# Performance work log

Hardware: AMD Instinct MI355X
Metric: run time of the kernel (lower is better)

## Reference

```python
import jax, jax.numpy as jnp
import numpy as np

B, S, C = 512, 16384, 3
CLASS_W = jnp.array([1.23954983922, 5.3172413793, 192.75], dtype=jnp.float32)


def setup_inputs() -> dict:
    key = jax.random.key(0)
    kx, kc, kl = jax.random.split(key, 3)
    x = jax.random.normal(kx, (B, S, C), dtype=jnp.float32)
    # one-hot labels with a random valid prefix length per sample (>=1);
    # rows beyond the length are all-zero (the module's padding sentinel [0,0,0])
    classes = jax.random.randint(kc, (B, S), 0, C)                      # [B,S]
    lengths = jax.random.randint(kl, (B,), 1, S + 1)                    # [B], 1..S
    valid = jnp.arange(S)[None, :] < lengths[:, None]                   # [B,S] bool
    label = jax.nn.one_hot(classes, C, dtype=jnp.int64) * valid[:, :, None]
    return {"x": x, "label": label}


def reference(x, label):
    # padding_index scan: first all-zero label row ends the valid prefix
    nonzero = jnp.any(label != 0, axis=-1)                              # [B,S]
    valid = jnp.cumprod(nonzero.astype(jnp.int32), axis=1)              # [B,S] 0/1 prefix mask
    valid_f = valid.astype(x.dtype)

    # weighted soft-target cross entropy per token:
    #   l_t = -sum_c w_c * y_{t,c} * log_softmax(x_t)_c
    logp = jax.nn.log_softmax(x, axis=-1)                               # [B,S,C]
    tok_loss = -jnp.einsum('bsc,c,bsc->bs', label.astype(x.dtype), CLASS_W, logp)

    # per-sample: mean over the valid prefix (CrossEntropyLoss mean over N
    # tokens for probability targets), then sum over the batch (python loop +=)
    n_valid = jnp.sum(valid_f, axis=1)                                  # [B]
    per_sample = jnp.sum(tok_loss * valid_f, axis=1) / n_valid          # [B]
    loss = jnp.sum(per_sample)
    return loss
```

## Files before the change

kernel.cpp:

```cpp
#include <hip/hip_runtime.h>


#define NB      512
#define NS      16384
#define NSPLIT  4
#define RPB     (NS / NSPLIT)
#define NTH     512
#define GRP     (RPB / 4)

__device__ __forceinline__ float row_loss(float xa, float xb, float xc,
                                          int la, int lb, int lc) {
    const float w0 = 1.23954983922f, w1 = 5.3172413793f, w2 = 192.75f;
    float m   = fmaxf(fmaxf(xa, xb), xc);
    float lse = m + __logf(__expf(xa - m) + __expf(xb - m) + __expf(xc - m));
    return w0 * (float)la * (lse - xa)
         + w1 * (float)lb * (lse - xb)
         + w2 * (float)lc * (lse - xc);
}

__global__ __launch_bounds__(NTH) void ls_partial(
    const float* __restrict__ x, const int* __restrict__ lab,
    float* __restrict__ psum, int* __restrict__ pcnt)
{
    const int blk = blockIdx.x;
    const int b   = blk & (NB - 1);
    const int sp  = blk >> 9;
    const long long base = ((long long)b * NS + (long long)sp * RPB) * 3;
    const int*   lr = lab + base;
    const float* xr = x   + base;

    int f0 = lr[0], f1 = lr[1], f2 = lr[2];
    int e0 = lr[(RPB - 1) * 3], e1 = lr[(RPB - 1) * 3 + 1], e2 = lr[(RPB - 1) * 3 + 2];

    if ((f0 | f1 | f2) == 0) {
        if (threadIdx.x == 0) { psum[blk] = 0.0f; pcnt[blk] = 0; }
        return;
    }

    float sumA = 0.0f, sumB = 0.0f;
    int   cnt = 0;

    if ((e0 | e1 | e2) != 0) {
        const int g0 = threadIdx.x;
        const int g1 = threadIdx.x + NTH;
        const int4*   lp0 = (const int4*)lr + (size_t)g0 * 3;
        const int4*   lp1 = (const int4*)lr + (size_t)g1 * 3;
        const float4* xp0 = (const float4*)xr + (size_t)g0 * 3;
        const float4* xp1 = (const float4*)xr + (size_t)g1 * 3;

        int4   a0 = lp0[0], a1 = lp0[1], a2 = lp0[2];
        int4   b0 = lp1[0], b1 = lp1[1], b2 = lp1[2];
        float4 u0 = xp0[0], u1 = xp0[1], u2 = xp0[2];
        float4 v0 = xp1[0], v1 = xp1[1], v2 = xp1[2];

        sumA += row_loss(u0.x, u0.y, u0.z, a0.x, a0.y, a0.z);
        sumB += row_loss(u0.w, u1.x, u1.y, a0.w, a1.x, a1.y);
        sumA += row_loss(u1.z, u1.w, u2.x, a1.z, a1.w, a2.x);
        sumB += row_loss(u2.y, u2.z, u2.w, a2.y, a2.z, a2.w);
        sumA += row_loss(v0.x, v0.y, v0.z, b0.x, b0.y, b0.z);
        sumB += row_loss(v0.w, v1.x, v1.y, b0.w, b1.x, b1.y);
        sumA += row_loss(v1.z, v1.w, v2.x, b1.z, b1.w, b2.x);
        sumB += row_loss(v2.y, v2.z, v2.w, b2.y, b2.z, b2.w);
        cnt = 8;
    } else {
        for (int g = threadIdx.x; g < GRP; g += NTH) {
            const int4* lp = (const int4*)lr + (size_t)g * 3;
            int4 l0 = lp[0], l1 = lp[1], l2 = lp[2];
            int any = l0.x | l0.y | l0.z | l0.w |
                      l1.x | l1.y | l1.z | l1.w |
                      l2.x | l2.y | l2.z | l2.w;
            if (any == 0) continue;
            const float4* xp = (const float4*)xr + (size_t)g * 3;
            float4 x0 = xp[0], x1 = xp[1], x2 = xp[2];
            float xv[12] = {x0.x, x0.y, x0.z, x0.w,
                            x1.x, x1.y, x1.z, x1.w,
                            x2.x, x2.y, x2.z, x2.w};
            int   lv[12] = {l0.x, l0.y, l0.z, l0.w,
                            l1.x, l1.y, l1.z, l1.w,
                            l2.x, l2.y, l2.z, l2.w};
#pragma unroll
            for (int r = 0; r < 4; ++r) {
                int la = lv[3*r], lb = lv[3*r+1], lc = lv[3*r+2];
                if ((la | lb | lc) == 0) continue;
                sumA += row_loss(xv[3*r], xv[3*r+1], xv[3*r+2], la, lb, lc);
                cnt += 1;
            }
        }
    }

    float sum = sumA + sumB;

#pragma unroll
    for (int off = 32; off > 0; off >>= 1) {
        sum += __shfl_down(sum, off);
        cnt += __shfl_down(cnt, off);
    }
    __shared__ float ssum[NTH / 64];
    __shared__ int   scnt[NTH / 64];
    const int lane = threadIdx.x & 63;
    const int wid  = threadIdx.x >> 6;
    if (lane == 0) { ssum[wid] = sum; scnt[wid] = cnt; }
    __syncthreads();
    if (threadIdx.x == 0) {
        float ts = 0.0f; int tc = 0;
#pragma unroll
        for (int i = 0; i < NTH / 64; ++i) { ts += ssum[i]; tc += scnt[i]; }
        psum[blk] = ts;
        pcnt[blk] = tc;
    }
}

__global__ __launch_bounds__(NB) void ls_final(
    const float* __restrict__ psum, const int* __restrict__ pcnt,
    float* __restrict__ out)
{
    const int b = threadIdx.x;
    float s = 0.0f; int c = 0;
#pragma unroll
    for (int i = 0; i < NSPLIT; ++i) {
        s += psum[i * NB + b];
        c += pcnt[i * NB + b];
    }
    float per = (c > 0) ? (s / (float)c) : 0.0f;

#pragma unroll
    for (int off = 32; off > 0; off >>= 1) per += __shfl_down(per, off);
    __shared__ float sh[NB / 64];
    const int lane = threadIdx.x & 63;
    const int wid  = threadIdx.x >> 6;
    if (lane == 0) sh[wid] = per;
    __syncthreads();
    if (threadIdx.x == 0) {
        float t = 0.0f;
#pragma unroll
        for (int i = 0; i < NB / 64; ++i) t += sh[i];
        out[0] = t;
    }
}

extern "C" void kernel_launch(void* const* d_in, const int* in_sizes, int n_in,
                              void* d_out, int out_size, void* d_ws, size_t ws_size,
                              hipStream_t stream)
{
    const float* x   = (const float*)d_in[0];
    const int*   lab = (const int*)d_in[1];

    float* psum = (float*)d_ws;
    int*   pcnt = (int*)((char*)d_ws + (size_t)NB * NSPLIT * sizeof(float));

    ls_partial<<<NB * NSPLIT, NTH, 0, stream>>>(x, lab, psum, pcnt);
    ls_final<<<1, NB, 0, stream>>>(psum, pcnt, (float*)d_out);
}
```

Baseline: 26.06 us.

## Split rows finer across blocks and make per-row masking branchless

Each sample's sequence is now split into 16 chunks instead of 4, with 256 threads per block. Every thread handles exactly four rows in a single vectorized load, so the separate full-chunk and partial-chunk code paths are gone. The valid-row count now comes from a branchless label-OR test per row, and the zero-count guard in the final reduction is removed. The aim is finer work distribution, more blocks that can exit early on padded chunks, and less divergence. The cost is that x is now loaded even for padded rows inside partially valid chunks, and there are more partial sums to write.

```diff
diff --git a/kernel.cpp b/kernel.cpp
--- a/kernel.cpp
+++ b/kernel.cpp
@@ -3,10 +3,10 @@
 
 #define NB      512
 #define NS      16384
-#define NSPLIT  4
+#define NSPLIT  16
 #define RPB     (NS / NSPLIT)
-#define NTH     512
-#define GRP     (RPB / 4)
+#define NTH     256
+#define NBLK    (NB * NSPLIT)
 
 __device__ __forceinline__ float row_loss(float xa, float xb, float xc,
                                           int la, int lb, int lc) {
@@ -30,66 +30,30 @@
     const float* xr = x   + base;
 
     int f0 = lr[0], f1 = lr[1], f2 = lr[2];
-    int e0 = lr[(RPB - 1) * 3], e1 = lr[(RPB - 1) * 3 + 1], e2 = lr[(RPB - 1) * 3 + 2];
-
     if ((f0 | f1 | f2) == 0) {
         if (threadIdx.x == 0) { psum[blk] = 0.0f; pcnt[blk] = 0; }
         return;
     }
 
+    const int g0 = threadIdx.x;
+    const int4*   lp0 = (const int4*)lr + (size_t)g0 * 3;
+    const float4* xp0 = (const float4*)xr + (size_t)g0 * 3;
+
+    int4   a0 = lp0[0], a1 = lp0[1], a2 = lp0[2];
+    float4 u0 = xp0[0], u1 = xp0[1], u2 = xp0[2];
+
     float sumA = 0.0f, sumB = 0.0f;
-    int   cnt = 0;
-
-    if ((e0 | e1 | e2) != 0) {
-        const int g0 = threadIdx.x;
-        const int g1 = threadIdx.x + NTH;
-        const int4*   lp0 = (const int4*)lr + (size_t)g0 * 3;
-        const int4*   lp1 = (const int4*)lr + (size_t)g1 * 3;
-        const float4* xp0 = (const float4*)xr + (size_t)g0 * 3;
-        const float4* xp1 = (const float4*)xr + (size_t)g1 * 3;
-
-        int4   a0 = lp0[0], a1 = lp0[1], a2 = lp0[2];
-        int4   b0 = lp1[0], b1 = lp1[1], b2 = lp1[2];
-        float4 u0 = xp0[0], u1 = xp0[1], u2 = xp0[2];
-        float4 v0 = xp1[0], v1 = xp1[1], v2 = xp1[2];
-
-        sumA += row_loss(u0.x, u0.y, u0.z, a0.x, a0.y, a0.z);
-        sumB += row_loss(u0.w, u1.x, u1.y, a0.w, a1.x, a1.y);
-        sumA += row_loss(u1.z, u1.w, u2.x, a1.z, a1.w, a2.x);
-        sumB += row_loss(u2.y, u2.z, u2.w, a2.y, a2.z, a2.w);
-        sumA += row_loss(v0.x, v0.y, v0.z, b0.x, b0.y, b0.z);
-        sumB += row_loss(v0.w, v1.x, v1.y, b0.w, b1.x, b1.y);
-        sumA += row_loss(v1.z, v1.w, v2.x, b1.z, b1.w, b2.x);
-        sumB += row_loss(v2.y, v2.z, v2.w, b2.y, b2.z, b2.w);
-        cnt = 8;
-    } else {
-        for (int g = threadIdx.x; g < GRP; g += NTH) {
-            const int4* lp = (const int4*)lr + (size_t)g * 3;
-            int4 l0 = lp[0], l1 = lp[1], l2 = lp[2];
-            int any = l0.x | l0.y | l0.z | l0.w |
-                      l1.x | l1.y | l1.z | l1.w |
-                      l2.x | l2.y | l2.z | l2.w;
-            if (any == 0) continue;
-            const float4* xp = (const float4*)xr + (size_t)g * 3;
-            float4 x0 = xp[0], x1 = xp[1], x2 = xp[2];
-            float xv[12] = {x0.x, x0.y, x0.z, x0.w,
-                            x1.x, x1.y, x1.z, x1.w,
-                            x2.x, x2.y, x2.z, x2.w};
-            int   lv[12] = {l0.x, l0.y, l0.z, l0.w,
-                            l1.x, l1.y, l1.z, l1.w,
-                            l2.x, l2.y, l2.z, l2.w};
-#pragma unroll
-            for (int r = 0; r < 4; ++r) {
-                int la = lv[3*r], lb = lv[3*r+1], lc = lv[3*r+2];
-                if ((la | lb | lc) == 0) continue;
-                sumA += row_loss(xv[3*r], xv[3*r+1], xv[3*r+2], la, lb, lc);
-                cnt += 1;
-            }
-        }
-    }
+    int   cnt  = 0;
+    sumA += row_loss(u0.x, u0.y, u0.z, a0.x, a0.y, a0.z);
+    cnt  += ((a0.x | a0.y | a0.z) != 0);
+    sumB += row_loss(u0.w, u1.x, u1.y, a0.w, a1.x, a1.y);
+    cnt  += ((a0.w | a1.x | a1.y) != 0);
+    sumA += row_loss(u1.z, u1.w, u2.x, a1.z, a1.w, a2.x);
+    cnt  += ((a1.z | a1.w | a2.x) != 0);
+    sumB += row_loss(u2.y, u2.z, u2.w, a2.y, a2.z, a2.w);
+    cnt  += ((a2.y | a2.z | a2.w) != 0);
 
     float sum = sumA + sumB;
-
 #pragma unroll
     for (int off = 32; off > 0; off >>= 1) {
         sum += __shfl_down(sum, off);
@@ -121,7 +85,7 @@
         s += psum[i * NB + b];
         c += pcnt[i * NB + b];
     }
-    float per = (c > 0) ? (s / (float)c) : 0.0f;
+    float per = s / (float)c;
 
 #pragma unroll
     for (int off = 32; off > 0; off >>= 1) per += __shfl_down(per, off);
@@ -146,8 +110,8 @@
     const int*   lab = (const int*)d_in[1];
 
     float* psum = (float*)d_ws;
-    int*   pcnt = (int*)((char*)d_ws + (size_t)NB * NSPLIT * sizeof(float));
+    int*   pcnt = (int*)((char*)d_ws + (size_t)NBLK * sizeof(float));
 
-    ls_partial<<<NB * NSPLIT, NTH, 0, stream>>>(x, lab, psum, pcnt);
+    ls_partial<<<NBLK, NTH, 0, stream>>>(x, lab, psum, pcnt);
     ls_final<<<1, NB, 0, stream>>>(psum, pcnt, (float*)d_out);
 }
```

Result: faster. 24.28 us (-6.8%).
